# Kernel tuning notes

Measured on AMD Instinct MI355X. Metric: run time of the kernel, lower is better.

The kernel has to match this reference:

```python
import jax, jax.numpy as jnp
import numpy as np

N_VERTS = 200_000
EMBD_D = 256
M_QUERIES = 500_000


def setup_inputs() -> dict:
    key = jax.random.key(0)
    ks = jax.random.split(key, 8)
    s = 1.0 / np.sqrt(EMBD_D)
    return {
        "p_vertices": jax.random.randint(ks[0], (M_QUERIES,), 0, N_VERTS, dtype=jnp.int64)
        if jax.config.jax_enable_x64 else jax.random.randint(ks[0], (M_QUERIES,), 0, N_VERTS, dtype=jnp.int32),
        "q_vertices": jax.random.randint(ks[1], (M_QUERIES,), 0, N_VERTS, dtype=jnp.int32),
        "embedding": jax.random.normal(ks[2], (N_VERTS, EMBD_D), dtype=jnp.float32),
        "w1": jax.random.normal(ks[3], (EMBD_D, EMBD_D), dtype=jnp.float32) * s,
        "b1": jnp.zeros((EMBD_D,), jnp.float32),
        "w2": jax.random.normal(ks[4], (EMBD_D, EMBD_D), dtype=jnp.float32) * s,
        "b2": jnp.zeros((EMBD_D,), jnp.float32),
        "w3": jax.random.normal(ks[5], (EMBD_D, 1), dtype=jnp.float32) * s,
        "b3": jnp.zeros((1,), jnp.float32),
    }


def reference(p_vertices, q_vertices, embedding, w1, b1, w2, b2, w3, b3):
    # gather two rows per query and take elementwise squared difference  [M, D]
    embd = (embedding[p_vertices] - embedding[q_vertices]) ** 2
    # small MLP decoder: 256 -> 256 -> 256 -> 1, ReLU activations
    h = jax.nn.relu(embd @ w1 + b1)
    h = jax.nn.relu(h @ w2 + b2)
    pred = (h @ w3 + b3).squeeze(-1)  # [M]
    return pred
```

## Files before the change

kernel.cpp:

```cpp
#include <hip/hip_runtime.h>
#include <hip/hip_bf16.h>
#include <stdint.h>


#define D 256
#define MT 128
#define THREADS 512

typedef __attribute__((ext_vector_type(8))) short short8;
typedef __attribute__((ext_vector_type(4))) float f32x4;

__device__ __forceinline__ unsigned short f2bf(float f) {
    unsigned int u = __float_as_uint(f);
    unsigned int r = (u + 0x7FFFu + ((u >> 16) & 1u)) >> 16;
    return (unsigned short)r;
}
__device__ __forceinline__ float bflo(unsigned int u) { return __uint_as_float(u << 16); }
__device__ __forceinline__ float bfhi(unsigned int u) { return __uint_as_float(u & 0xFFFF0000u); }

__device__ __forceinline__ unsigned int sqdiff2(unsigned int p, unsigned int q) {
    float d0 = bflo(p) - bflo(q);
    float d1 = bfhi(p) - bfhi(q);
    return (unsigned int)f2bf(d0 * d0) | ((unsigned int)f2bf(d1 * d1) << 16);
}

__global__ void conv_emb_kernel(const float* __restrict__ in,
                                unsigned short* __restrict__ out, int nchunks) {
    int i = blockIdx.x * blockDim.x + threadIdx.x;
    if (i >= nchunks) return;
    const float4* p = reinterpret_cast<const float4*>(in) + 2 * (size_t)i;
    float4 a = p[0], b = p[1];
    uint4 o;
    o.x = (unsigned int)f2bf(a.x) | ((unsigned int)f2bf(a.y) << 16);
    o.y = (unsigned int)f2bf(a.z) | ((unsigned int)f2bf(a.w) << 16);
    o.z = (unsigned int)f2bf(b.x) | ((unsigned int)f2bf(b.y) << 16);
    o.w = (unsigned int)f2bf(b.z) | ((unsigned int)f2bf(b.w) << 16);
    reinterpret_cast<uint4*>(out)[i] = o;
}

__global__ void pack_w_kernel(const float* __restrict__ w1,
                              const float* __restrict__ w2,
                              unsigned short* __restrict__ out) {
    int tid = blockIdx.x * blockDim.x + threadIdx.x;
    int mat = tid >> 13;
    const float* W = mat ? w2 : w1;
    unsigned short* o = out + mat * 65536;
    int rem  = tid & 8191;
    int nt   = rem >> 9;
    int ks   = (rem >> 6) & 7;
    int lane = rem & 63;
    int kbase = ks * 32 + (lane >> 4) * 8;
    int n     = nt * 16 + (lane & 15);
    short8 v;
#pragma unroll
    for (int j = 0; j < 8; ++j)
        v[j] = (short)f2bf(W[(kbase + j) * 256 + n]);
    *reinterpret_cast<short8*>(o + (((nt * 8) + ks) * 64 + lane) * 8) = v;
}

template <bool BF16T>
__launch_bounds__(THREADS, 2)
__global__ void fused_kernel(const int* __restrict__ pv,
                             const int* __restrict__ qv,
                             const float* __restrict__ embf,
                             const unsigned short* __restrict__ embb,
                             const float* __restrict__ b1,
                             const float* __restrict__ b2,
                             const float* __restrict__ w3,
                             const float* __restrict__ b3,
                             const unsigned short* __restrict__ wpack,
                             float* __restrict__ out,
                             int M) {
    __shared__ unsigned char lds_a[MT * 512];
    __shared__ float lds_part[4][MT];

    const int tid  = threadIdx.x;
    const int lane = tid & 63;
    const int wave = tid >> 6;
    const int base = blockIdx.x * MT;

    if (BF16T) {
#pragma unroll
        for (int it = 0; it < 8; ++it) {
            int r  = wave * 16 + it * 2 + (lane >> 5);
            int gi = base + r;
            int pi = 0, qi = 0;
            if (gi < M) { pi = pv[gi]; qi = qv[gi]; }
            int c = lane & 31;
            uint4 a = *(reinterpret_cast<const uint4*>(embb + (size_t)pi * D) + c);
            uint4 b = *(reinterpret_cast<const uint4*>(embb + (size_t)qi * D) + c);
            uint4 o;
            o.x = sqdiff2(a.x, b.x);
            o.y = sqdiff2(a.y, b.y);
            o.z = sqdiff2(a.z, b.z);
            o.w = sqdiff2(a.w, b.w);
            unsigned int unit = (unsigned int)c ^ (unsigned int)(r & 31);
            *reinterpret_cast<uint4*>(&lds_a[(unsigned int)r * 512u + (unit << 4)]) = o;
        }
    } else {
#pragma unroll
        for (int rr = 0; rr < 16; ++rr) {
            int r  = wave * 16 + rr;
            int gi = base + r;
            int pi = 0, qi = 0;
            if (gi < M) { pi = pv[gi]; qi = qv[gi]; }
            const float4* ep = reinterpret_cast<const float4*>(embf + (size_t)pi * D);
            const float4* eq = reinterpret_cast<const float4*>(embf + (size_t)qi * D);
            float4 a = ep[lane];
            float4 b = eq[lane];
            float d0 = a.x - b.x, d1 = a.y - b.y, d2 = a.z - b.z, d3 = a.w - b.w;
            unsigned int lo = (unsigned int)f2bf(d0 * d0) | ((unsigned int)f2bf(d1 * d1) << 16);
            unsigned int hi = (unsigned int)f2bf(d2 * d2) | ((unsigned int)f2bf(d3 * d3) << 16);
            unsigned int unit = (unsigned int)(lane >> 1) ^ (unsigned int)(r & 31);
            unsigned int addr = (unsigned int)r * 512u + (unit << 4) + (unsigned int)(lane & 1) * 8u;
            *reinterpret_cast<uint2*>(&lds_a[addr]) = make_uint2(lo, hi);
        }
    }
    __syncthreads();

    const int wm    = wave & 1;
    const int wn    = wave >> 1;
    const int mbase = wm * 64;
    const int nbase = wn * 64;
    const int l15   = lane & 15;
    const int quad  = lane >> 4;

    const short8* wp1 = reinterpret_cast<const short8*>(wpack);
    const short8* wp2 = reinterpret_cast<const short8*>(wpack + 65536);

    f32x4 acc[4][4];
    short8 bfr[4][8];

#pragma unroll
    for (int ct = 0; ct < 4; ++ct) {
        int ntg = (nbase >> 4) + ct;
#pragma unroll
        for (int ks = 0; ks < 8; ++ks)
            bfr[ct][ks] = wp1[((ntg * 8) + ks) * 64 + lane];
    }
#pragma unroll
    for (int mt = 0; mt < 4; ++mt)
#pragma unroll
        for (int ct = 0; ct < 4; ++ct)
            acc[mt][ct] = (f32x4){0.f, 0.f, 0.f, 0.f};

#pragma unroll
    for (int ks = 0; ks < 8; ++ks) {
        short8 af[4];
#pragma unroll
        for (int mt = 0; mt < 4; ++mt) {
            int r = mbase + mt * 16 + l15;
            unsigned int unit = (unsigned int)(ks * 4 + quad) ^ (unsigned int)(r & 31);
            af[mt] = *reinterpret_cast<const short8*>(&lds_a[(unsigned int)r * 512u + (unit << 4)]);
        }
#pragma unroll
        for (int mt = 0; mt < 4; ++mt)
#pragma unroll
            for (int ct = 0; ct < 4; ++ct)
                acc[mt][ct] = __builtin_amdgcn_mfma_f32_16x16x32_bf16(
                    af[mt], bfr[ct][ks], acc[mt][ct], 0, 0, 0);
    }

    __syncthreads();

#pragma unroll
    for (int ct = 0; ct < 4; ++ct) {
        int c = nbase + ct * 16 + l15;
        float bias = b1[c];
#pragma unroll
        for (int mt = 0; mt < 4; ++mt) {
#pragma unroll
            for (int j = 0; j < 4; ++j) {
                float v = acc[mt][ct][j] + bias;
                v = fmaxf(v, 0.f);
                int r = mbase + mt * 16 + quad * 4 + j;
                unsigned int unit = (unsigned int)(c >> 3) ^ (unsigned int)(r & 31);
                unsigned int addr = (unsigned int)r * 512u + (unit << 4) + (unsigned int)(c & 7) * 2u;
                *reinterpret_cast<unsigned short*>(&lds_a[addr]) = f2bf(v);
            }
        }
    }
    __syncthreads();

#pragma unroll
    for (int ct = 0; ct < 4; ++ct) {
        int ntg = (nbase >> 4) + ct;
#pragma unroll
        for (int ks = 0; ks < 8; ++ks)
            bfr[ct][ks] = wp2[((ntg * 8) + ks) * 64 + lane];
    }
#pragma unroll
    for (int mt = 0; mt < 4; ++mt)
#pragma unroll
        for (int ct = 0; ct < 4; ++ct)
            acc[mt][ct] = (f32x4){0.f, 0.f, 0.f, 0.f};

#pragma unroll
    for (int ks = 0; ks < 8; ++ks) {
        short8 af[4];
#pragma unroll
        for (int mt = 0; mt < 4; ++mt) {
            int r = mbase + mt * 16 + l15;
            unsigned int unit = (unsigned int)(ks * 4 + quad) ^ (unsigned int)(r & 31);
            af[mt] = *reinterpret_cast<const short8*>(&lds_a[(unsigned int)r * 512u + (unit << 4)]);
        }
#pragma unroll
        for (int mt = 0; mt < 4; ++mt)
#pragma unroll
            for (int ct = 0; ct < 4; ++ct)
                acc[mt][ct] = __builtin_amdgcn_mfma_f32_16x16x32_bf16(
                    af[mt], bfr[ct][ks], acc[mt][ct], 0, 0, 0);
    }

    float part[4][4];
#pragma unroll
    for (int mt = 0; mt < 4; ++mt)
#pragma unroll
        for (int j = 0; j < 4; ++j)
            part[mt][j] = 0.f;

#pragma unroll
    for (int ct = 0; ct < 4; ++ct) {
        int c = nbase + ct * 16 + l15;
        float bias = b2[c];
        float w3v  = w3[c];
#pragma unroll
        for (int mt = 0; mt < 4; ++mt)
#pragma unroll
            for (int j = 0; j < 4; ++j) {
                float v = acc[mt][ct][j] + bias;
                v = fmaxf(v, 0.f);
                part[mt][j] += v * w3v;
            }
    }

#pragma unroll
    for (int msk = 8; msk >= 1; msk >>= 1)
#pragma unroll
        for (int mt = 0; mt < 4; ++mt)
#pragma unroll
            for (int j = 0; j < 4; ++j)
                part[mt][j] += __shfl_xor(part[mt][j], msk, 64);

    if (l15 == 0) {
#pragma unroll
        for (int mt = 0; mt < 4; ++mt)
#pragma unroll
            for (int j = 0; j < 4; ++j) {
                int r = mbase + mt * 16 + quad * 4 + j;
                lds_part[wn][r] = part[mt][j];
            }
    }
    __syncthreads();

    if (tid < MT) {
        int gi = base + tid;
        if (gi < M) {
            float s = lds_part[0][tid] + lds_part[1][tid] +
                      lds_part[2][tid] + lds_part[3][tid] + b3[0];
            out[gi] = s;
        }
    }
}

extern "C" void kernel_launch(void* const* d_in, const int* in_sizes, int n_in,
                              void* d_out, int out_size, void* d_ws, size_t ws_size,
                              hipStream_t stream) {
    const int*   pv  = (const int*)d_in[0];
    const int*   qv  = (const int*)d_in[1];
    const float* emb = (const float*)d_in[2];
    const float* w1  = (const float*)d_in[3];
    const float* b1  = (const float*)d_in[4];
    const float* w2  = (const float*)d_in[5];
    const float* b2  = (const float*)d_in[6];
    const float* w3  = (const float*)d_in[7];
    const float* b3  = (const float*)d_in[8];
    float* out = (float*)d_out;
    const int M  = in_sizes[0];
    const int NV = in_sizes[2] / D;

    const size_t tbl_bytes   = (size_t)NV * D * sizeof(unsigned short);
    const size_t wpack_bytes = 2u * 65536u * sizeof(unsigned short);
    const bool use_bf16 = (ws_size >= tbl_bytes + wpack_bytes);

    unsigned short* table = (unsigned short*)d_ws;
    unsigned short* wpack = use_bf16
        ? (unsigned short*)((char*)d_ws + tbl_bytes)
        : (unsigned short*)d_ws;

    pack_w_kernel<<<32, 512, 0, stream>>>(w1, w2, wpack);

    int nblk = (M + MT - 1) / MT;
    if (use_bf16) {
        int nch = (int)((size_t)NV * D / 8);
        conv_emb_kernel<<<(nch + 255) / 256, 256, 0, stream>>>(emb, table, nch);
        fused_kernel<true><<<nblk, THREADS, 0, stream>>>(
            pv, qv, emb, table, b1, b2, w3, b3, wpack, out, M);
    } else {
        fused_kernel<false><<<nblk, THREADS, 0, stream>>>(
            pv, qv, emb, nullptr, b1, b2, w3, b3, wpack, out, M);
    }
}
```

Measured before the change: 603.5 us.

## Halve block tile to 64 rows and double-buffer weight fragments per k-step

Shrinks each block to 64 query rows and 4 waves, each wave covering all 64 rows for its 64 output columns, and raises launch bounds to 3 blocks per SIMD group. Instead of preloading all 32 weight fragments per wave into registers, weights are streamed two k-steps ahead with a ping-pong buffer. This cuts register use and LDS per block to raise occupancy and hide the gather latency. The cost is more global/L2 weight traffic per query, since each weight tile is now reused across fewer rows.

Result: faster. 513.7 us (-14.9%).

```diff
diff --git a/kernel.cpp b/kernel.cpp
--- a/kernel.cpp
+++ b/kernel.cpp
@@ -4,8 +4,8 @@
 
 
 #define D 256
-#define MT 128
-#define THREADS 512
+#define MT 64
+#define THREADS 256
 
 typedef __attribute__((ext_vector_type(8))) short short8;
 typedef __attribute__((ext_vector_type(4))) float f32x4;
@@ -59,7 +59,7 @@
 }
 
 template <bool BF16T>
-__launch_bounds__(THREADS, 2)
+__launch_bounds__(THREADS, 3)
 __global__ void fused_kernel(const int* __restrict__ pv,
                              const int* __restrict__ qv,
                              const float* __restrict__ embf,
@@ -118,9 +118,7 @@
     }
     __syncthreads();
 
-    const int wm    = wave & 1;
-    const int wn    = wave >> 1;
-    const int mbase = wm * 64;
+    const int wn    = wave;
     const int nbase = wn * 64;
     const int l15   = lane & 15;
     const int quad  = lane >> 4;
@@ -129,36 +127,49 @@
     const short8* wp2 = reinterpret_cast<const short8*>(wpack + 65536);
 
     f32x4 acc[4][4];
-    short8 bfr[4][8];
-
-#pragma unroll
-    for (int ct = 0; ct < 4; ++ct) {
-        int ntg = (nbase >> 4) + ct;
-#pragma unroll
-        for (int ks = 0; ks < 8; ++ks)
-            bfr[ct][ks] = wp1[((ntg * 8) + ks) * 64 + lane];
-    }
+    short8 bb0[4], bb1[4];
+
+#define LOADB(buf, wp, ksv)                                            \
+    _Pragma("unroll")                                                  \
+    for (int ct = 0; ct < 4; ++ct)                                     \
+        buf[ct] = (wp)[((((nbase >> 4) + ct) * 8) + (ksv)) * 64 + lane];
+
+#define LOADA(af, ksv)                                                               \
+    _Pragma("unroll")                                                                \
+    for (int mt = 0; mt < 4; ++mt) {                                                 \
+        int r = mt * 16 + l15;                                                       \
+        unsigned int unit = (unsigned int)((ksv) * 4 + quad) ^ (unsigned int)(r & 31);\
+        af[mt] = *reinterpret_cast<const short8*>(                                   \
+            &lds_a[(unsigned int)r * 512u + (unit << 4)]);                           \
+    }
+
+#define MFMA16(bu)                                                      \
+    _Pragma("unroll")                                                   \
+    for (int mt = 0; mt < 4; ++mt)                                      \
+        _Pragma("unroll")                                               \
+        for (int ct = 0; ct < 4; ++ct)                                  \
+            acc[mt][ct] = __builtin_amdgcn_mfma_f32_16x16x32_bf16(      \
+                af[mt], bu[ct], acc[mt][ct], 0, 0, 0);
+
 #pragma unroll
     for (int mt = 0; mt < 4; ++mt)
 #pragma unroll
         for (int ct = 0; ct < 4; ++ct)
             acc[mt][ct] = (f32x4){0.f, 0.f, 0.f, 0.f};
 
+    LOADB(bb0, wp1, 0)
+    LOADB(bb1, wp1, 1)
 #pragma unroll
     for (int ks = 0; ks < 8; ++ks) {
         short8 af[4];
-#pragma unroll
-        for (int mt = 0; mt < 4; ++mt) {
-            int r = mbase + mt * 16 + l15;
-            unsigned int unit = (unsigned int)(ks * 4 + quad) ^ (unsigned int)(r & 31);
-            af[mt] = *reinterpret_cast<const short8*>(&lds_a[(unsigned int)r * 512u + (unit << 4)]);
-        }
-#pragma unroll
-        for (int mt = 0; mt < 4; ++mt)
-#pragma unroll
-            for (int ct = 0; ct < 4; ++ct)
-                acc[mt][ct] = __builtin_amdgcn_mfma_f32_16x16x32_bf16(
-                    af[mt], bfr[ct][ks], acc[mt][ct], 0, 0, 0);
+        LOADA(af, ks)
+        if (ks & 1) {
+            MFMA16(bb1)
+            if (ks + 2 < 8) LOADB(bb1, wp1, ks + 2)
+        } else {
+            MFMA16(bb0)
+            if (ks + 2 < 8) LOADB(bb0, wp1, ks + 2)
+        }
     }
 
     __syncthreads();
@@ -173,7 +184,7 @@
             for (int j = 0; j < 4; ++j) {
                 float v = acc[mt][ct][j] + bias;
                 v = fmaxf(v, 0.f);
-                int r = mbase + mt * 16 + quad * 4 + j;
+                int r = mt * 16 + quad * 4 + j;
                 unsigned int unit = (unsigned int)(c >> 3) ^ (unsigned int)(r & 31);
                 unsigned int addr = (unsigned int)r * 512u + (unit << 4) + (unsigned int)(c & 7) * 2u;
                 *reinterpret_cast<unsigned short*>(&lds_a[addr]) = f2bf(v);
@@ -183,33 +194,24 @@
     __syncthreads();
 
 #pragma unroll
-    for (int ct = 0; ct < 4; ++ct) {
-        int ntg = (nbase >> 4) + ct;
-#pragma unroll
-        for (int ks = 0; ks < 8; ++ks)
-            bfr[ct][ks] = wp2[((ntg * 8) + ks) * 64 + lane];
-    }
-#pragma unroll
     for (int mt = 0; mt < 4; ++mt)
 #pragma unroll
         for (int ct = 0; ct < 4; ++ct)
             acc[mt][ct] = (f32x4){0.f, 0.f, 0.f, 0.f};
 
+    LOADB(bb0, wp2, 0)
+    LOADB(bb1, wp2, 1)
 #pragma unroll
     for (int ks = 0; ks < 8; ++ks) {
         short8 af[4];
-#pragma unroll
-        for (int mt = 0; mt < 4; ++mt) {
-            int r = mbase + mt * 16 + l15;
-            unsigned int unit = (unsigned int)(ks * 4 + quad) ^ (unsigned int)(r & 31);
-            af[mt] = *reinterpret_cast<const short8*>(&lds_a[(unsigned int)r * 512u + (unit << 4)]);
-        }
-#pragma unroll
-        for (int mt = 0; mt < 4; ++mt)
-#pragma unroll
-            for (int ct = 0; ct < 4; ++ct)
-                acc[mt][ct] = __builtin_amdgcn_mfma_f32_16x16x32_bf16(
-                    af[mt], bfr[ct][ks], acc[mt][ct], 0, 0, 0);
+        LOADA(af, ks)
+        if (ks & 1) {
+            MFMA16(bb1)
+            if (ks + 2 < 8) LOADB(bb1, wp2, ks + 2)
+        } else {
+            MFMA16(bb0)
+            if (ks + 2 < 8) LOADB(bb0, wp2, ks + 2)
+        }
     }
 
     float part[4][4];
@@ -247,7 +249,7 @@
         for (int mt = 0; mt < 4; ++mt)
 #pragma unroll
             for (int j = 0; j < 4; ++j) {
-                int r = mbase + mt * 16 + quad * 4 + j;
+                int r = mt * 16 + quad * 4 + j;
                 lds_part[wn][r] = part[mt][j];
             }
     }
```

## Make fused MLP kernel persistent with register-resident weights and double-buffered gather

Applied to the files above, without the earlier changes.

Turns the fused kernel into a persistent grid-stride loop over 64-row tiles with 256 threads. Both layer weight fragments stay in registers for the whole loop, and the next tile's embedding gather is issued into registers and committed to a second LDS buffer while the current tile's GEMMs run. This removes the per-block reloading of weights and hides gather latency behind MFMA work. The cost is heavy register pressure from holding both weight sets plus the prefetch buffers, which risks spilling or low occupancy, and a fixed grid of 512 blocks.

Result: slower. 1.157 ms (+91.8%).

```diff
diff --git a/kernel.cpp b/kernel.cpp
--- a/kernel.cpp
+++ b/kernel.cpp
@@ -4,8 +4,9 @@
 
 
 #define D 256
-#define MT 128
-#define THREADS 512
+#define MT 64
+#define THREADS 256
+#define PGRID 512
 
 typedef __attribute__((ext_vector_type(8))) short short8;
 typedef __attribute__((ext_vector_type(4))) float f32x4;
@@ -70,196 +71,194 @@
                              const float* __restrict__ b3,
                              const unsigned short* __restrict__ wpack,
                              float* __restrict__ out,
-                             int M) {
-    __shared__ unsigned char lds_a[MT * 512];
+                             int M, int nblk) {
+    __shared__ unsigned char lds_a[2][MT * 512];
     __shared__ float lds_part[4][MT];
 
     const int tid  = threadIdx.x;
     const int lane = tid & 63;
     const int wave = tid >> 6;
-    const int base = blockIdx.x * MT;
-
-    if (BF16T) {
+    const int rr   = lane >> 5;
+    const int cc   = lane & 31;
+    const int l15  = lane & 15;
+    const int quad = lane >> 4;
+    const int nbase = wave * 64;
+
+    const short8* wp = reinterpret_cast<const short8*>(wpack);
+    short8 wb1[4][8], wb2[4][8];
+#pragma unroll
+    for (int ct = 0; ct < 4; ++ct)
+#pragma unroll
+        for (int ks = 0; ks < 8; ++ks) {
+            int fi = ((((nbase >> 4) + ct) * 8) + ks) * 64 + lane;
+            wb1[ct][ks] = wp[fi];
+            wb2[ct][ks] = wp[8192 + fi];
+        }
+    float b1v[4], b2v[4], w3v[4];
+#pragma unroll
+    for (int ct = 0; ct < 4; ++ct) {
+        int c = nbase + ct * 16 + l15;
+        b1v[ct] = b1[c];
+        b2v[ct] = b2[c];
+        w3v[ct] = w3[c];
+    }
+    const float b3v = b3[0];
+
+    auto issue_gather = [&](int t, uint4* ga, uint4* gb) {
 #pragma unroll
         for (int it = 0; it < 8; ++it) {
-            int r  = wave * 16 + it * 2 + (lane >> 5);
-            int gi = base + r;
+            int r  = wave * 16 + it * 2 + rr;
+            int gi = t * MT + r;
             int pi = 0, qi = 0;
             if (gi < M) { pi = pv[gi]; qi = qv[gi]; }
-            int c = lane & 31;
-            uint4 a = *(reinterpret_cast<const uint4*>(embb + (size_t)pi * D) + c);
-            uint4 b = *(reinterpret_cast<const uint4*>(embb + (size_t)qi * D) + c);
+            ga[it] = *(reinterpret_cast<const uint4*>(embb + (size_t)pi * D) + cc);
+            gb[it] = *(reinterpret_cast<const uint4*>(embb + (size_t)qi * D) + cc);
+        }
+    };
+    auto commit_gather = [&](const uint4* ga, const uint4* gb, unsigned char* buf) {
+#pragma unroll
+        for (int it = 0; it < 8; ++it) {
+            int r = wave * 16 + it * 2 + rr;
             uint4 o;
-            o.x = sqdiff2(a.x, b.x);
-            o.y = sqdiff2(a.y, b.y);
-            o.z = sqdiff2(a.z, b.z);
-            o.w = sqdiff2(a.w, b.w);
-            unsigned int unit = (unsigned int)c ^ (unsigned int)(r & 31);
-            *reinterpret_cast<uint4*>(&lds_a[(unsigned int)r * 512u + (unit << 4)]) = o;
-        }
-    } else {
-#pragma unroll
-        for (int rr = 0; rr < 16; ++rr) {
-            int r  = wave * 16 + rr;
-            int gi = base + r;
+            o.x = sqdiff2(ga[it].x, gb[it].x);
+            o.y = sqdiff2(ga[it].y, gb[it].y);
+            o.z = sqdiff2(ga[it].z, gb[it].z);
+            o.w = sqdiff2(ga[it].w, gb[it].w);
+            unsigned int unit = (unsigned int)cc ^ (unsigned int)(r & 31);
+            *reinterpret_cast<uint4*>(&buf[(unsigned int)r * 512u + (unit << 4)]) = o;
+        }
+    };
+    auto gather_fp32 = [&](int t, unsigned char* buf) {
+#pragma unroll
+        for (int it = 0; it < 8; ++it) {
+            int r  = wave * 16 + it * 2 + rr;
+            int gi = t * MT + r;
             int pi = 0, qi = 0;
             if (gi < M) { pi = pv[gi]; qi = qv[gi]; }
-            const float4* ep = reinterpret_cast<const float4*>(embf + (size_t)pi * D);
-            const float4* eq = reinterpret_cast<const float4*>(embf + (size_t)qi * D);
-            float4 a = ep[lane];
-            float4 b = eq[lane];
-            float d0 = a.x - b.x, d1 = a.y - b.y, d2 = a.z - b.z, d3 = a.w - b.w;
-            unsigned int lo = (unsigned int)f2bf(d0 * d0) | ((unsigned int)f2bf(d1 * d1) << 16);
-            unsigned int hi = (unsigned int)f2bf(d2 * d2) | ((unsigned int)f2bf(d3 * d3) << 16);
-            unsigned int unit = (unsigned int)(lane >> 1) ^ (unsigned int)(r & 31);
-            unsigned int addr = (unsigned int)r * 512u + (unit << 4) + (unsigned int)(lane & 1) * 8u;
-            *reinterpret_cast<uint2*>(&lds_a[addr]) = make_uint2(lo, hi);
-        }
-    }
+            const float4* ep = reinterpret_cast<const float4*>(embf + (size_t)pi * D) + cc * 2;
+            const float4* eq = reinterpret_cast<const float4*>(embf + (size_t)qi * D) + cc * 2;
+            float4 a0 = ep[0], a1 = ep[1], q0 = eq[0], q1 = eq[1];
+            float d0 = a0.x - q0.x, d1 = a0.y - q0.y, d2 = a0.z - q0.z, d3 = a0.w - q0.w;
+            float d4 = a1.x - q1.x, d5 = a1.y - q1.y, d6 = a1.z - q1.z, d7 = a1.w - q1.w;
+            uint4 o;
+            o.x = (unsigned int)f2bf(d0 * d0) | ((unsigned int)f2bf(d1 * d1) << 16);
+            o.y = (unsigned int)f2bf(d2 * d2) | ((unsigned int)f2bf(d3 * d3) << 16);
+            o.z = (unsigned int)f2bf(d4 * d4) | ((unsigned int)f2bf(d5 * d5) << 16);
+            o.w = (unsigned int)f2bf(d6 * d6) | ((unsigned int)f2bf(d7 * d7) << 16);
+            unsigned int unit = (unsigned int)cc ^ (unsigned int)(r & 31);
+            *reinterpret_cast<uint4*>(&buf[(unsigned int)r * 512u + (unit << 4)]) = o;
+        }
+    };
+    auto gemm = [&](const short8 (&wbg)[4][8], const unsigned char* buf,
+                    f32x4 (&acc)[4][4]) {
+#pragma unroll
+        for (int mt = 0; mt < 4; ++mt)
+#pragma unroll
+            for (int ct = 0; ct < 4; ++ct)
+                acc[mt][ct] = (f32x4){0.f, 0.f, 0.f, 0.f};
+#pragma unroll
+        for (int ks = 0; ks < 8; ++ks) {
+            short8 af[4];
+#pragma unroll
+            for (int mt = 0; mt < 4; ++mt) {
+                int r = mt * 16 + l15;
+                unsigned int unit = (unsigned int)(ks * 4 + quad) ^ (unsigned int)(r & 31);
+                af[mt] = *reinterpret_cast<const short8*>(
+                    &buf[(unsigned int)r * 512u + (unit << 4)]);
+            }
+#pragma unroll
+            for (int mt = 0; mt < 4; ++mt)
+#pragma unroll
+                for (int ct = 0; ct < 4; ++ct)
+                    acc[mt][ct] = __builtin_amdgcn_mfma_f32_16x16x32_bf16(
+                        af[mt], wbg[ct][ks], acc[mt][ct], 0, 0, 0);
+        }
+    };
+
+    const int stride = gridDim.x;
+    int t = blockIdx.x;
+    if (t >= nblk) return;
+
+    uint4 ga[8], gb[8];
+    int cur = 0;
+
+    if (BF16T) { issue_gather(t, ga, gb); commit_gather(ga, gb, lds_a[0]); }
+    else       { gather_fp32(t, lds_a[0]); }
     __syncthreads();
 
-    const int wm    = wave & 1;
-    const int wn    = wave >> 1;
-    const int mbase = wm * 64;
-    const int nbase = wn * 64;
-    const int l15   = lane & 15;
-    const int quad  = lane >> 4;
-
-    const short8* wp1 = reinterpret_cast<const short8*>(wpack);
-    const short8* wp2 = reinterpret_cast<const short8*>(wpack + 65536);
-
-    f32x4 acc[4][4];
-    short8 bfr[4][8];
-
-#pragma unroll
-    for (int ct = 0; ct < 4; ++ct) {
-        int ntg = (nbase >> 4) + ct;
-#pragma unroll
-        for (int ks = 0; ks < 8; ++ks)
-            bfr[ct][ks] = wp1[((ntg * 8) + ks) * 64 + lane];
-    }
-#pragma unroll
-    for (int mt = 0; mt < 4; ++mt)
+    for (; t < nblk; t += stride) {
+        const int  tn = t + stride;
+        const bool hn = (tn < nblk);
+
+        if (BF16T && hn) issue_gather(tn, ga, gb);
+
+        f32x4 acc[4][4];
+        gemm(wb1, lds_a[cur], acc);
+        __syncthreads();
+
+#pragma unroll
+        for (int ct = 0; ct < 4; ++ct) {
+            int c = nbase + ct * 16 + l15;
+#pragma unroll
+            for (int mt = 0; mt < 4; ++mt)
+#pragma unroll
+                for (int j = 0; j < 4; ++j) {
+                    float v = fmaxf(acc[mt][ct][j] + b1v[ct], 0.f);
+                    int r = mt * 16 + quad * 4 + j;
+                    unsigned int unit = (unsigned int)(c >> 3) ^ (unsigned int)(r & 31);
+                    unsigned int addr = (unsigned int)r * 512u + (unit << 4)
+                                      + (unsigned int)(c & 7) * 2u;
+                    *reinterpret_cast<unsigned short*>(&lds_a[cur][addr]) = f2bf(v);
+                }
+        }
+        __syncthreads();
+
+        gemm(wb2, lds_a[cur], acc);
+
+        float part[4][4];
+#pragma unroll
+        for (int mt = 0; mt < 4; ++mt)
+#pragma unroll
+            for (int j = 0; j < 4; ++j)
+                part[mt][j] = 0.f;
 #pragma unroll
         for (int ct = 0; ct < 4; ++ct)
-            acc[mt][ct] = (f32x4){0.f, 0.f, 0.f, 0.f};
-
-#pragma unroll
-    for (int ks = 0; ks < 8; ++ks) {
-        short8 af[4];
-#pragma unroll
-        for (int mt = 0; mt < 4; ++mt) {
-            int r = mbase + mt * 16 + l15;
-            unsigned int unit = (unsigned int)(ks * 4 + quad) ^ (unsigned int)(r & 31);
-            af[mt] = *reinterpret_cast<const short8*>(&lds_a[(unsigned int)r * 512u + (unit << 4)]);
-        }
-#pragma unroll
-        for (int mt = 0; mt < 4; ++mt)
-#pragma unroll
-            for (int ct = 0; ct < 4; ++ct)
-                acc[mt][ct] = __builtin_amdgcn_mfma_f32_16x16x32_bf16(
-                    af[mt], bfr[ct][ks], acc[mt][ct], 0, 0, 0);
-    }
-
-    __syncthreads();
-
-#pragma unroll
-    for (int ct = 0; ct < 4; ++ct) {
-        int c = nbase + ct * 16 + l15;
-        float bias = b1[c];
-#pragma unroll
-        for (int mt = 0; mt < 4; ++mt) {
-#pragma unroll
-            for (int j = 0; j < 4; ++j) {
-                float v = acc[mt][ct][j] + bias;
-                v = fmaxf(v, 0.f);
-                int r = mbase + mt * 16 + quad * 4 + j;
-                unsigned int unit = (unsigned int)(c >> 3) ^ (unsigned int)(r & 31);
-                unsigned int addr = (unsigned int)r * 512u + (unit << 4) + (unsigned int)(c & 7) * 2u;
-                *reinterpret_cast<unsigned short*>(&lds_a[addr]) = f2bf(v);
+#pragma unroll
+            for (int mt = 0; mt < 4; ++mt)
+#pragma unroll
+                for (int j = 0; j < 4; ++j) {
+                    float v = fmaxf(acc[mt][ct][j] + b2v[ct], 0.f);
+                    part[mt][j] += v * w3v[ct];
+                }
+#pragma unroll
+        for (int msk = 8; msk >= 1; msk >>= 1)
+#pragma unroll
+            for (int mt = 0; mt < 4; ++mt)
+#pragma unroll
+                for (int j = 0; j < 4; ++j)
+                    part[mt][j] += __shfl_xor(part[mt][j], msk, 64);
+        if (l15 == 0) {
+#pragma unroll
+            for (int mt = 0; mt < 4; ++mt)
+#pragma unroll
+                for (int j = 0; j < 4; ++j)
+                    lds_part[wave][mt * 16 + quad * 4 + j] = part[mt][j];
+        }
+
+        if (hn) {
+            if (BF16T) commit_gather(ga, gb, lds_a[cur ^ 1]);
+            else       gather_fp32(tn, lds_a[cur ^ 1]);
+        }
+        __syncthreads();
+
+        if (tid < MT) {
+            int gi = t * MT + tid;
+            if (gi < M) {
+                out[gi] = lds_part[0][tid] + lds_part[1][tid] +
+                          lds_part[2][tid] + lds_part[3][tid] + b3v;
             }
         }
-    }
-    __syncthreads();
-
-#pragma unroll
-    for (int ct = 0; ct < 4; ++ct) {
-        int ntg = (nbase >> 4) + ct;
-#pragma unroll
-        for (int ks = 0; ks < 8; ++ks)
-            bfr[ct][ks] = wp2[((ntg * 8) + ks) * 64 + lane];
-    }
-#pragma unroll
-    for (int mt = 0; mt < 4; ++mt)
-#pragma unroll
-        for (int ct = 0; ct < 4; ++ct)
-            acc[mt][ct] = (f32x4){0.f, 0.f, 0.f, 0.f};
-
-#pragma unroll
-    for (int ks = 0; ks < 8; ++ks) {
-        short8 af[4];
-#pragma unroll
-        for (int mt = 0; mt < 4; ++mt) {
-            int r = mbase + mt * 16 + l15;
-            unsigned int unit = (unsigned int)(ks * 4 + quad) ^ (unsigned int)(r & 31);
-            af[mt] = *reinterpret_cast<const short8*>(&lds_a[(unsigned int)r * 512u + (unit << 4)]);
-        }
-#pragma unroll
-        for (int mt = 0; mt < 4; ++mt)
-#pragma unroll
-            for (int ct = 0; ct < 4; ++ct)
-                acc[mt][ct] = __builtin_amdgcn_mfma_f32_16x16x32_bf16(
-                    af[mt], bfr[ct][ks], acc[mt][ct], 0, 0, 0);
-    }
-
-    float part[4][4];
-#pragma unroll
-    for (int mt = 0; mt < 4; ++mt)
-#pragma unroll
-        for (int j = 0; j < 4; ++j)
-            part[mt][j] = 0.f;
-
-#pragma unroll
-    for (int ct = 0; ct < 4; ++ct) {
-        int c = nbase + ct * 16 + l15;
-        float bias = b2[c];
-        float w3v  = w3[c];
-#pragma unroll
-        for (int mt = 0; mt < 4; ++mt)
-#pragma unroll
-            for (int j = 0; j < 4; ++j) {
-                float v = acc[mt][ct][j] + bias;
-                v = fmaxf(v, 0.f);
-                part[mt][j] += v * w3v;
-            }
-    }
-
-#pragma unroll
-    for (int msk = 8; msk >= 1; msk >>= 1)
-#pragma unroll
-        for (int mt = 0; mt < 4; ++mt)
-#pragma unroll
-            for (int j = 0; j < 4; ++j)
-                part[mt][j] += __shfl_xor(part[mt][j], msk, 64);
-
-    if (l15 == 0) {
-#pragma unroll
-        for (int mt = 0; mt < 4; ++mt)
-#pragma unroll
-            for (int j = 0; j < 4; ++j) {
-                int r = mbase + mt * 16 + quad * 4 + j;
-                lds_part[wn][r] = part[mt][j];
-            }
-    }
-    __syncthreads();
-
-    if (tid < MT) {
-        int gi = base + tid;
-        if (gi < M) {
-            float s = lds_part[0][tid] + lds_part[1][tid] +
-                      lds_part[2][tid] + lds_part[3][tid] + b3[0];
-            out[gi] = s;
-        }
+        cur ^= 1;
     }
 }
 
@@ -290,14 +289,15 @@
 
     pack_w_kernel<<<32, 512, 0, stream>>>(w1, w2, wpack);
 
-    int nblk = (M + MT - 1) / MT;
+    const int nblk = (M + MT - 1) / MT;
+    const int grid = nblk < PGRID ? nblk : PGRID;
     if (use_bf16) {
         int nch = (int)((size_t)NV * D / 8);
         conv_emb_kernel<<<(nch + 255) / 256, 256, 0, stream>>>(emb, table, nch);
-        fused_kernel<true><<<nblk, THREADS, 0, stream>>>(
-            pv, qv, emb, table, b1, b2, w3, b3, wpack, out, M);
+        fused_kernel<true><<<grid, THREADS, 0, stream>>>(
+            pv, qv, emb, table, b1, b2, w3, b3, wpack, out, M, nblk);
     } else {
-        fused_kernel<false><<<nblk, THREADS, 0, stream>>>(
-            pv, qv, emb, nullptr, b1, b2, w3, b3, wpack, out, M);
+        fused_kernel<false><<<grid, THREADS, 0, stream>>>(
+            pv, qv, emb, nullptr, b1, b2, w3, b3, wpack, out, M, nblk);
     }
 }
```
